# Kernel tuning notes

Measured on AMD Instinct MI355X. Metric: run time of the kernel, lower is better.

The kernel has to match this reference:

```python
import jax, jax.numpy as jnp
import numpy as np
from jax import lax

B, CIN, COUT, K, S, P, H, W = 8, 128, 256, 3, 1, 1, 64, 64


def setup_inputs() -> dict:
    key = jax.random.key(0)
    k1, k2, k3, k4, k5 = jax.random.split(key, 5)
    fan_off = CIN * K * K
    fan_dc = CIN * K * K
    return {
        "x": jax.random.normal(k1, (B, CIN, H, W), dtype=jnp.float32),
        # offset-predicting conv: Conv2d(CIN, 2*K*K, K, S, P, padding_mode='reflect')
        "w_off": jax.random.normal(k2, (2 * K * K, CIN, K, K), dtype=jnp.float32) / np.sqrt(fan_off),
        "b_off": jax.random.normal(k3, (2 * K * K,), dtype=jnp.float32) * 0.01,
        # deformable conv weights: DeformConv2d(CIN, COUT, K, S, P)
        "w_dc": jax.random.normal(k4, (COUT, CIN, K, K), dtype=jnp.float32) / np.sqrt(fan_dc),
        "b_dc": jax.random.normal(k5, (COUT,), dtype=jnp.float32) * 0.01,
    }


def _reflect_conv(x, w, b, stride, pad):
    # Conv2d with reflect padding
    xp = jnp.pad(x, ((0, 0), (0, 0), (pad, pad), (pad, pad)), mode="reflect")
    y = lax.conv_general_dilated(xp, w, (stride, stride), "VALID",
                                 dimension_numbers=("NCHW", "OIHW", "NCHW"))
    return y + b[None, :, None, None]


def _deform_conv(x, offset, w, b, k, stride, pad):
    # torchvision DeformConv2d (v1, no mask, 1 offset group)
    Bn, C, Hi, Wi = x.shape
    Ho, Wo = offset.shape[2], offset.shape[3]
    KK = k * k
    # offset layout: [B, 2*KK, Ho, Wo], interleaved (dy, dx) per kernel position
    off = offset.reshape(Bn, KK, 2, Ho, Wo)
    hb = jnp.arange(Ho, dtype=x.dtype) * stride - pad          # base rows
    wb = jnp.arange(Wo, dtype=x.dtype) * stride - pad          # base cols
    ki, kj = jnp.meshgrid(jnp.arange(k, dtype=x.dtype), jnp.arange(k, dtype=x.dtype), indexing="ij")
    ki, kj = ki.reshape(KK), kj.reshape(KK)
    # sampling locations [B, KK, Ho, Wo]
    py = off[:, :, 0] + hb[None, None, :, None] + ki[None, :, None, None]
    px = off[:, :, 1] + wb[None, None, None, :] + kj[None, :, None, None]
    y0 = jnp.floor(py)
    x0 = jnp.floor(px)
    dy = (py - y0).reshape(Bn, 1, -1)
    dx = (px - x0).reshape(Bn, 1, -1)
    y0i = y0.astype(jnp.int32)
    x0i = x0.astype(jnp.int32)
    xf = x.reshape(Bn, C, Hi * Wi)

    def gather(yi, xi):
        valid = (yi >= 0) & (yi < Hi) & (xi >= 0) & (xi < Wi)
        yc = jnp.clip(yi, 0, Hi - 1)
        xc = jnp.clip(xi, 0, Wi - 1)
        idx = (yc * Wi + xc).reshape(Bn, -1)                   # [B, KK*Ho*Wo]
        g = jax.vmap(lambda xb, ib: xb[:, ib])(xf, idx)        # [B, C, KK*Ho*Wo]
        return g * valid.reshape(Bn, 1, -1).astype(x.dtype)

    v00 = gather(y0i, x0i)
    v01 = gather(y0i, x0i + 1)
    v10 = gather(y0i + 1, x0i)
    v11 = gather(y0i + 1, x0i + 1)
    vals = (v00 * (1 - dy) * (1 - dx) + v01 * (1 - dy) * dx
            + v10 * dy * (1 - dx) + v11 * dy * dx)             # [B, C, KK*Ho*Wo]
    cols = vals.reshape(Bn, C, KK, Ho * Wo)
    out = jnp.einsum("bckl,ock->bol", cols, w.reshape(-1, C, KK))
    out = out + b[None, :, None]
    return out.reshape(Bn, -1, Ho, Wo)


def reference(x, w_off, b_off, w_dc, b_dc):
    x_offset = _reflect_conv(x, w_off, b_off, S, P)            # [B, 2*K*K, Ho, Wo]
    # torch.chunk followed by torch.concat is an identity on the offset tensor
    return _deform_conv(x, x_offset, w_dc, b_dc, K, S, P)
```

## Files before the change

### kernel.cpp

```cpp
#include <hip/hip_runtime.h>
#include <hip/hip_fp16.h>

typedef unsigned short u16;
typedef unsigned int   u32;
typedef u32   u32x2  __attribute__((ext_vector_type(2)));
typedef u32   u32x4  __attribute__((ext_vector_type(4)));
typedef short short8 __attribute__((ext_vector_type(8)));
typedef float f32x4  __attribute__((ext_vector_type(4)));
typedef _Float16 half8 __attribute__((ext_vector_type(8)));

__device__ __forceinline__ u16 f2h(float f) { return __half_as_ushort(__float2half(f)); }
__device__ __forceinline__ f32x4 mfma16(short8 a, short8 b, f32x4 c) {
  return __builtin_amdgcn_mfma_f32_16x16x32_f16(
      __builtin_bit_cast(half8, a), __builtin_bit_cast(half8, b), c, 0, 0, 0);
}
__device__ __forceinline__ __half2 h2cast(u32 u) { return __builtin_bit_cast(__half2, u); }

__global__ __launch_bounds__(256) void prep_fused(const float* __restrict__ x,
                                                  const float* __restrict__ w_dc,
                                                  const float* __restrict__ w_off,
                                                  u16* __restrict__ xh,
                                                  u16* __restrict__ Wl2,
                                                  u16* __restrict__ Wol2) {
  int bid = blockIdx.x;
  int tid = threadIdx.x;
  if (bid < 512) {
    __shared__ float tile[128][65];
    int swz = (bid & 7) * 64 + (bid >> 3);
    int b = swz >> 6, h = swz & 63;
    for (int i = 0; i < 32; ++i) {
      int c = (tid >> 6) + i * 4;
      int w = tid & 63;
      tile[c][w] = x[(((size_t)b * 128 + c) * 64 + h) * 64 + w];
    }
    __syncthreads();
    u16* dst = xh + ((size_t)(b * 64 + h) * 64) * 128;
    for (int j = 0; j < 32; ++j) {
      int c = tid & 127;
      int w = (tid >> 7) + 2 * j;
      dst[w * 128 + c] = f2h(tile[c][w]);
    }
  } else {
    int idx = (bid - 512) * 256 + tid;
    if (idx < 294912) {
      int e = idx & 7, lane = (idx >> 3) & 63, ks = (idx >> 9) & 3;
      int mt = (idx >> 11) & 15, kk = idx >> 15;
      int o = mt * 16 + (lane & 15), c = ks * 32 + (lane >> 4) * 8 + e;
      Wl2[idx] = f2h(w_dc[(o * 128 + c) * 9 + kk]);
    } else {
      int i2 = idx - 294912;
      int e = i2 & 7, lane = (i2 >> 3) & 63, ks = (i2 >> 9) & 3;
      int mt = (i2 >> 11) & 1, kk = i2 >> 12;
      int co = mt * 16 + (lane & 15), c = ks * 32 + (lane >> 4) * 8 + e;
      Wol2[i2] = (co < 18) ? f2h(w_off[(co * 128 + c) * 9 + kk]) : (u16)0;
    }
  }
}

__device__ __forceinline__ void make_entry_lds(u32x4* __restrict__ tbl, int kk,
                                               int ho, int wo, float offy, float offx) {
  int ki = kk / 3, kj = kk - ki * 3;
  float py = offy + (float)(ho + ki - 1);
  float px = offx + (float)(wo + kj - 1);
  float fy0 = floorf(py), fx0 = floorf(px);
  int y0 = (int)fy0, x0 = (int)fx0;
  float fy = py - fy0, fx = px - fx0;
  float w11 = fy * fx, w10 = fy - w11, w01 = fx - w11, w00 = 1.f - fy - fx + w11;
  bool iy0 = (y0 >= 0) & (y0 < 64), iy1 = (y0 >= -1) & (y0 < 63);
  bool ix0 = (x0 >= 0) & (x0 < 64), ix1 = (x0 >= -1) & (x0 < 63);
  int y0c = min(max(y0, 0), 63), x0c = min(max(x0, 0), 63);
  u32 addr00 = (u32)((y0c * 64 + x0c) * 128);
  u32 dx = (x0 >= 0 && x0 < 63) ? 128u : 0u;
  u32 dy = (y0 >= 0 && y0 < 63) ? 8192u : 0u;
  u32 wA = (u32)f2h((iy0 && ix0) ? w00 : 0.f) | ((u32)f2h((iy0 && ix1) ? w01 : 0.f) << 16);
  u32 wB = (u32)f2h((iy1 && ix0) ? w10 : 0.f) | ((u32)f2h((iy1 && ix1) ? w11 : 0.f) << 16);
  u32x4 ent; ent.x = addr00; ent.y = dx | (dy << 16); ent.z = wA; ent.w = wB;
  tbl[kk * 64 + wo] = ent;
}

__global__ __launch_bounds__(512, 4) void deform_fused(
    const u16* __restrict__ xh, const u16* __restrict__ Wl2,
    const u16* __restrict__ Wol2, const float* __restrict__ b_off,
    const float* __restrict__ b_dc, float* __restrict__ out) {
  union SMU {
    u16 slab[3][64][128];
    struct { u16 cols[2][64][128]; u32x4 tbl[576]; } pb;
  };
  __shared__ SMU sm;
  int bid = blockIdx.x;
  int swz = (bid & 7) * 64 + (bid >> 3);
  int b = swz >> 6, ho = swz & 63;
  int tid = threadIdx.x, lane = tid & 63, wv = tid >> 6;
  int ln15 = lane & 15, kg = lane >> 4;
  const u16* xb = xh + (size_t)b * 524288;

  int tl0 = tid >> 4;
  int tcl = (tid & 15) * 8;
  int swzc = tcl ^ ((tl0 & 7) << 3);

  {
    u32x4 st[6];
#pragma unroll
    for (int i = 0; i < 6; ++i) {
      int T = tid + i * 512;
      int r = T >> 10, w = (T >> 4) & 63, cb = (T & 15) * 8;
      int hr = ho + r - 1; hr = hr < 0 ? -hr : (hr > 63 ? 126 - hr : hr);
      st[i] = *(const u32x4*)(xb + (hr * 64 + w) * 128 + cb);
    }
#pragma unroll
    for (int i = 0; i < 6; ++i) {
      int T = tid + i * 512;
      int r = T >> 10, w = (T >> 4) & 63, cb = (T & 15) * 8;
      *(u32x4*)&sm.slab[r][w][cb ^ ((w & 7) << 3)] = st[i];
    }
  }
  __syncthreads();

  int mt = wv & 1, ntq = wv >> 1;
  int lq = ntq * 16 + ln15;
  f32x4 oacc = {0.f, 0.f, 0.f, 0.f};
  __builtin_amdgcn_s_setprio(1);
#pragma unroll
  for (int kk = 0; kk < 9; ++kk) {
    int ki = kk / 3, kj = kk - ki * 3;
    int wr = lq + kj - 1; wr = wr < 0 ? -wr : (wr > 63 ? 126 - wr : wr);
    const u16* wb = Wol2 + ((kk * 2 + mt) * 4) * 512 + lane * 8;
    int sb = (wr & 7) << 3;
#pragma unroll
    for (int ks = 0; ks < 4; ++ks) {
      short8 af = *(const short8*)(wb + ks * 512);
      short8 bf = *(const short8*)&sm.slab[ki][wr][(ks * 32 + kg * 8) ^ sb];
      oacc = mfma16(af, bf, oacc);
    }
  }
  __builtin_amdgcn_s_setprio(0);
  __syncthreads();

  {
    int wo = lq;
    if (mt == 0) {
      int kkA = 2 * kg, kkB = 2 * kg + 1;
      make_entry_lds(sm.pb.tbl, kkA, ho, wo, oacc[0] + b_off[2 * kkA], oacc[1] + b_off[2 * kkA + 1]);
      make_entry_lds(sm.pb.tbl, kkB, ho, wo, oacc[2] + b_off[2 * kkB], oacc[3] + b_off[2 * kkB + 1]);
    } else if (kg == 0) {
      make_entry_lds(sm.pb.tbl, 8, ho, wo, oacc[0] + b_off[16], oacc[1] + b_off[17]);
    }
  }
  __syncthreads();

  u32x4 gv[2][4];
  u32x4 ge[2];
  auto gissue = [&](int g) {
#pragma unroll
    for (int i = 0; i < 2; ++i) {
      int l = tl0 + i * 32;
      u32x4 e = sm.pb.tbl[g * 64 + l];
      ge[i] = e;
      const u16* p = xb + e.x + tcl;
      u32 dxv = e.y & 0xffffu, dyv = e.y >> 16;
      gv[i][0] = *(const u32x4*)p;
      gv[i][1] = *(const u32x4*)(p + dxv);
      gv[i][2] = *(const u32x4*)(p + dyv);
      gv[i][3] = *(const u32x4*)(p + dyv + dxv);
    }
  };
  auto gwrite = [&](int dbuf) {
#pragma unroll
    for (int i = 0; i < 2; ++i) {
      __half2 wA = h2cast(ge[i].z), wB = h2cast(ge[i].w);
      __half2 w00 = __half2half2(wA.x), w01 = __half2half2(wA.y);
      __half2 w10 = __half2half2(wB.x), w11 = __half2half2(wB.y);
      u32x4 pv;
#pragma unroll
      for (int wd = 0; wd < 4; ++wd) {
        __half2 r = __hmul2(h2cast(gv[i][0][wd]), w00);
        r = __hfma2(h2cast(gv[i][1][wd]), w01, r);
        r = __hfma2(h2cast(gv[i][2][wd]), w10, r);
        r = __hfma2(h2cast(gv[i][3][wd]), w11, r);
        pv[wd] = __builtin_bit_cast(u32, r);
      }
      *(u32x4*)&sm.pb.cols[dbuf][tl0 + i * 32][swzc] = pv;
    }
  };

  f32x4 acc[2][4];
#pragma unroll
  for (int m = 0; m < 2; ++m)
#pragma unroll
    for (int n = 0; n < 4; ++n) acc[m][n] = (f32x4){0.f, 0.f, 0.f, 0.f};

  gissue(0);
  gwrite(0);
  __syncthreads();

  for (int kk = 0; kk < 9; ++kk) {
    int buf = kk & 1;
    const u16* wbase = Wl2 + (size_t)((kk * 16 + wv * 2) * 4) * 512;
    short8 a[8];
#pragma unroll
    for (int ks = 0; ks < 4; ++ks) {
      a[ks]     = *(const short8*)(wbase + ks * 512 + lane * 8);
      a[4 + ks] = *(const short8*)(wbase + (4 + ks) * 512 + lane * 8);
    }
    if (kk < 8) gissue(kk + 1);
    __builtin_amdgcn_s_setprio(1);
#pragma unroll
    for (int ks = 0; ks < 4; ++ks) {
#pragma unroll
      for (int nt = 0; nt < 4; ++nt) {
        int l = nt * 16 + ln15;
        short8 bfv = *(const short8*)&sm.pb.cols[buf][l][(ks * 32 + kg * 8) ^ ((l & 7) << 3)];
        acc[0][nt] = mfma16(a[ks], bfv, acc[0][nt]);
        acc[1][nt] = mfma16(a[4 + ks], bfv, acc[1][nt]);
      }
    }
    __builtin_amdgcn_s_setprio(0);
    if (kk < 8) gwrite(buf ^ 1);
    __syncthreads();
  }

#pragma unroll
  for (int mtt = 0; mtt < 2; ++mtt) {
#pragma unroll
    for (int r = 0; r < 4; ++r) {
      int o = wv * 32 + mtt * 16 + kg * 4 + r;
      float bias = b_dc[o];
      size_t base = ((size_t)(b * 256 + o)) * 4096 + ho * 64;
#pragma unroll
      for (int nt = 0; nt < 4; ++nt) {
        out[base + nt * 16 + ln15] = acc[mtt][nt][r] + bias;
      }
    }
  }
}

extern "C" void kernel_launch(void* const* d_in, const int* in_sizes, int n_in,
                              void* d_out, int out_size, void* d_ws, size_t ws_size,
                              hipStream_t stream) {
  const float* x     = (const float*)d_in[0];
  const float* w_off = (const float*)d_in[1];
  const float* b_off = (const float*)d_in[2];
  const float* w_dc  = (const float*)d_in[3];
  const float* b_dc  = (const float*)d_in[4];
  float* out = (float*)d_out;
  char* ws = (char*)d_ws;
  u16* xh   = (u16*)ws;
  u16* Wl2  = (u16*)(ws + 8388608);
  u16* Wol2 = (u16*)(ws + 8388608 + 589824);
  prep_fused  <<<dim3(1808), dim3(256), 0, stream>>>(x, w_dc, w_off, xh, Wl2, Wol2);
  deform_fused<<<dim3(512),  dim3(512), 0, stream>>>(xh, Wl2, Wol2, b_off, b_dc, out);
}
```

Measured before the change: 47.61 us.

## Halve workgroup to 256 threads with larger per-wave MFMA tiles and compact gather table

Changes the deform kernel from 512 to 256 threads per block, so each wave now computes 64 output channels (4 M-tiles) instead of 32. This reuses each LDS B-fragment across four MFMAs, and the offset conv now handles two N-tiles per wave. The gather/interpolation pipeline is split into two half-K phases per kernel tap to bound register use. The sampling table is packed into 3 words per entry instead of 4, and the batch-major block swizzle is replaced by a simple interleave. The aim is less LDS read traffic and a smaller LDS footprint, at the cost of fewer waves per block and higher register pressure from 64 accumulators per thread.

```diff
diff --git a/kernel.cpp b/kernel.cpp
--- a/kernel.cpp
+++ b/kernel.cpp
@@ -57,8 +57,8 @@
   }
 }
 
-__device__ __forceinline__ void make_entry_lds(u32x4* __restrict__ tbl, int kk,
-                                               int ho, int wo, float offy, float offx) {
+__device__ __forceinline__ void make_entry3(u32* __restrict__ tbl, int kk,
+                                            int ho, int wo, float offy, float offx) {
   int ki = kk / 3, kj = kk - ki * 3;
   float py = offy + (float)(ho + ki - 1);
   float px = offx + (float)(wo + kj - 1);
@@ -69,27 +69,28 @@
   bool iy0 = (y0 >= 0) & (y0 < 64), iy1 = (y0 >= -1) & (y0 < 63);
   bool ix0 = (x0 >= 0) & (x0 < 64), ix1 = (x0 >= -1) & (x0 < 63);
   int y0c = min(max(y0, 0), 63), x0c = min(max(x0, 0), 63);
-  u32 addr00 = (u32)((y0c * 64 + x0c) * 128);
-  u32 dx = (x0 >= 0 && x0 < 63) ? 128u : 0u;
-  u32 dy = (y0 >= 0 && y0 < 63) ? 8192u : 0u;
+  u32 addr = (u32)((y0c * 64 + x0c) * 128);
+  u32 dxf = (x0 >= 0 && x0 < 63) ? 1u : 0u;
+  u32 dyf = (y0 >= 0 && y0 < 63) ? 1u : 0u;
   u32 wA = (u32)f2h((iy0 && ix0) ? w00 : 0.f) | ((u32)f2h((iy0 && ix1) ? w01 : 0.f) << 16);
   u32 wB = (u32)f2h((iy1 && ix0) ? w10 : 0.f) | ((u32)f2h((iy1 && ix1) ? w11 : 0.f) << 16);
-  u32x4 ent; ent.x = addr00; ent.y = dx | (dy << 16); ent.z = wA; ent.w = wB;
-  tbl[kk * 64 + wo] = ent;
-}
-
-__global__ __launch_bounds__(512, 4) void deform_fused(
+  int base = (kk * 64 + wo) * 3;
+  tbl[base]     = addr | (dxf << 20) | (dyf << 21);
+  tbl[base + 1] = wA;
+  tbl[base + 2] = wB;
+}
+
+__global__ __launch_bounds__(256, 3) void deform_fused(
     const u16* __restrict__ xh, const u16* __restrict__ Wl2,
     const u16* __restrict__ Wol2, const float* __restrict__ b_off,
     const float* __restrict__ b_dc, float* __restrict__ out) {
   union SMU {
     u16 slab[3][64][128];
-    struct { u16 cols[2][64][128]; u32x4 tbl[576]; } pb;
+    struct { u16 cols[2][64][128]; u32 tbl[1728]; } pb;
   };
   __shared__ SMU sm;
   int bid = blockIdx.x;
-  int swz = (bid & 7) * 64 + (bid >> 3);
-  int b = swz >> 6, ho = swz & 63;
+  int b = bid & 7, ho = bid >> 3;
   int tid = threadIdx.x, lane = tid & 63, wv = tid >> 6;
   int ln15 = lane & 15, kg = lane >> 4;
   const u16* xb = xh + (size_t)b * 524288;
@@ -99,75 +100,81 @@
   int swzc = tcl ^ ((tl0 & 7) << 3);
 
   {
-    u32x4 st[6];
-#pragma unroll
-    for (int i = 0; i < 6; ++i) {
-      int T = tid + i * 512;
+    u32x4 st[12];
+#pragma unroll
+    for (int i = 0; i < 12; ++i) {
+      int T = tid + i * 256;
       int r = T >> 10, w = (T >> 4) & 63, cb = (T & 15) * 8;
       int hr = ho + r - 1; hr = hr < 0 ? -hr : (hr > 63 ? 126 - hr : hr);
       st[i] = *(const u32x4*)(xb + (hr * 64 + w) * 128 + cb);
     }
 #pragma unroll
-    for (int i = 0; i < 6; ++i) {
-      int T = tid + i * 512;
+    for (int i = 0; i < 12; ++i) {
+      int T = tid + i * 256;
       int r = T >> 10, w = (T >> 4) & 63, cb = (T & 15) * 8;
       *(u32x4*)&sm.slab[r][w][cb ^ ((w & 7) << 3)] = st[i];
     }
   }
   __syncthreads();
 
-  int mt = wv & 1, ntq = wv >> 1;
-  int lq = ntq * 16 + ln15;
-  f32x4 oacc = {0.f, 0.f, 0.f, 0.f};
+  int mtA = wv & 1;
+  int ntb = (wv >> 1) * 2;
+  int lqa = ntb * 16 + ln15, lqb = (ntb + 1) * 16 + ln15;
+  f32x4 oacc0 = {0.f, 0.f, 0.f, 0.f}, oacc1 = {0.f, 0.f, 0.f, 0.f};
   __builtin_amdgcn_s_setprio(1);
 #pragma unroll
   for (int kk = 0; kk < 9; ++kk) {
     int ki = kk / 3, kj = kk - ki * 3;
-    int wr = lq + kj - 1; wr = wr < 0 ? -wr : (wr > 63 ? 126 - wr : wr);
-    const u16* wb = Wol2 + ((kk * 2 + mt) * 4) * 512 + lane * 8;
-    int sb = (wr & 7) << 3;
+    int wra = lqa + kj - 1; wra = wra < 0 ? -wra : (wra > 63 ? 126 - wra : wra);
+    int wrb = lqb + kj - 1; wrb = wrb < 0 ? -wrb : (wrb > 63 ? 126 - wrb : wrb);
+    const u16* wb = Wol2 + ((kk * 2 + mtA) * 4) * 512 + lane * 8;
+    int sba = (wra & 7) << 3, sbb = (wrb & 7) << 3;
 #pragma unroll
     for (int ks = 0; ks < 4; ++ks) {
       short8 af = *(const short8*)(wb + ks * 512);
-      short8 bf = *(const short8*)&sm.slab[ki][wr][(ks * 32 + kg * 8) ^ sb];
-      oacc = mfma16(af, bf, oacc);
+      oacc0 = mfma16(af, *(const short8*)&sm.slab[ki][wra][(ks * 32 + kg * 8) ^ sba], oacc0);
+      oacc1 = mfma16(af, *(const short8*)&sm.slab[ki][wrb][(ks * 32 + kg * 8) ^ sbb], oacc1);
     }
   }
   __builtin_amdgcn_s_setprio(0);
   __syncthreads();
 
-  {
-    int wo = lq;
-    if (mt == 0) {
-      int kkA = 2 * kg, kkB = 2 * kg + 1;
-      make_entry_lds(sm.pb.tbl, kkA, ho, wo, oacc[0] + b_off[2 * kkA], oacc[1] + b_off[2 * kkA + 1]);
-      make_entry_lds(sm.pb.tbl, kkB, ho, wo, oacc[2] + b_off[2 * kkB], oacc[3] + b_off[2 * kkB + 1]);
-    } else if (kg == 0) {
-      make_entry_lds(sm.pb.tbl, 8, ho, wo, oacc[0] + b_off[16], oacc[1] + b_off[17]);
-    }
+  if (mtA == 0) {
+    int kkA = 2 * kg, kkB = 2 * kg + 1;
+    make_entry3(sm.pb.tbl, kkA, ho, lqa, oacc0[0] + b_off[2 * kkA], oacc0[1] + b_off[2 * kkA + 1]);
+    make_entry3(sm.pb.tbl, kkB, ho, lqa, oacc0[2] + b_off[2 * kkB], oacc0[3] + b_off[2 * kkB + 1]);
+    make_entry3(sm.pb.tbl, kkA, ho, lqb, oacc1[0] + b_off[2 * kkA], oacc1[1] + b_off[2 * kkA + 1]);
+    make_entry3(sm.pb.tbl, kkB, ho, lqb, oacc1[2] + b_off[2 * kkB], oacc1[3] + b_off[2 * kkB + 1]);
+  } else if (kg == 0) {
+    make_entry3(sm.pb.tbl, 8, ho, lqa, oacc0[0] + b_off[16], oacc0[1] + b_off[17]);
+    make_entry3(sm.pb.tbl, 8, ho, lqb, oacc1[0] + b_off[16], oacc1[1] + b_off[17]);
   }
   __syncthreads();
 
   u32x4 gv[2][4];
-  u32x4 ge[2];
-  auto gissue = [&](int g) {
+  u32 gwAv[2], gwBv[2];
+  auto gissue2 = [&](int g, int i0) {
 #pragma unroll
     for (int i = 0; i < 2; ++i) {
-      int l = tl0 + i * 32;
-      u32x4 e = sm.pb.tbl[g * 64 + l];
-      ge[i] = e;
-      const u16* p = xb + e.x + tcl;
-      u32 dxv = e.y & 0xffffu, dyv = e.y >> 16;
+      int l = tl0 + (i0 + i) * 16;
+      int base3 = (g * 64 + l) * 3;
+      u32 e0 = sm.pb.tbl[base3];
+      gwAv[i] = sm.pb.tbl[base3 + 1];
+      gwBv[i] = sm.pb.tbl[base3 + 2];
+      const u16* p = xb + (e0 & 0xFFFFFu) + tcl;
+      u32 dxv = ((e0 >> 20) & 1) << 7;
+      u32 dyv = ((e0 >> 21) & 1) << 13;
       gv[i][0] = *(const u32x4*)p;
       gv[i][1] = *(const u32x4*)(p + dxv);
       gv[i][2] = *(const u32x4*)(p + dyv);
       gv[i][3] = *(const u32x4*)(p + dyv + dxv);
     }
   };
-  auto gwrite = [&](int dbuf) {
+  auto gwrite2 = [&](int dbuf, int i0) {
 #pragma unroll
     for (int i = 0; i < 2; ++i) {
-      __half2 wA = h2cast(ge[i].z), wB = h2cast(ge[i].w);
+      int l = tl0 + (i0 + i) * 16;
+      __half2 wA = h2cast(gwAv[i]), wB = h2cast(gwBv[i]);
       __half2 w00 = __half2half2(wA.x), w01 = __half2half2(wA.y);
       __half2 w10 = __half2half2(wB.x), w11 = __half2half2(wB.y);
       u32x4 pv;
@@ -179,56 +186,78 @@
         r = __hfma2(h2cast(gv[i][3][wd]), w11, r);
         pv[wd] = __builtin_bit_cast(u32, r);
       }
-      *(u32x4*)&sm.pb.cols[dbuf][tl0 + i * 32][swzc] = pv;
+      *(u32x4*)&sm.pb.cols[dbuf][l][swzc] = pv;
     }
   };
 
-  f32x4 acc[2][4];
-#pragma unroll
-  for (int m = 0; m < 2; ++m)
+  f32x4 acc[4][4];
+#pragma unroll
+  for (int m = 0; m < 4; ++m)
 #pragma unroll
     for (int n = 0; n < 4; ++n) acc[m][n] = (f32x4){0.f, 0.f, 0.f, 0.f};
 
-  gissue(0);
-  gwrite(0);
-  __syncthreads();
-
+  gissue2(0, 0); gwrite2(0, 0);
+  gissue2(0, 2); gwrite2(0, 2);
+  __syncthreads();
+
+  int swzb = (ln15 & 7) << 3;
   for (int kk = 0; kk < 9; ++kk) {
     int buf = kk & 1;
-    const u16* wbase = Wl2 + (size_t)((kk * 16 + wv * 2) * 4) * 512;
-    short8 a[8];
-#pragma unroll
-    for (int ks = 0; ks < 4; ++ks) {
-      a[ks]     = *(const short8*)(wbase + ks * 512 + lane * 8);
-      a[4 + ks] = *(const short8*)(wbase + (4 + ks) * 512 + lane * 8);
-    }
-    if (kk < 8) gissue(kk + 1);
+    bool more = kk < 8;
+    const u16* wbase = Wl2 + (size_t)((kk * 16 + wv * 4) * 4) * 512 + lane * 8;
+    short8 a0[4][2];
+#pragma unroll
+    for (int mt = 0; mt < 4; ++mt)
+#pragma unroll
+      for (int k2 = 0; k2 < 2; ++k2)
+        a0[mt][k2] = *(const short8*)(wbase + (mt * 4 + k2) * 512);
+    if (more) gissue2(kk + 1, 0);
     __builtin_amdgcn_s_setprio(1);
 #pragma unroll
-    for (int ks = 0; ks < 4; ++ks) {
+    for (int k2 = 0; k2 < 2; ++k2) {
 #pragma unroll
       for (int nt = 0; nt < 4; ++nt) {
-        int l = nt * 16 + ln15;
-        short8 bfv = *(const short8*)&sm.pb.cols[buf][l][(ks * 32 + kg * 8) ^ ((l & 7) << 3)];
-        acc[0][nt] = mfma16(a[ks], bfv, acc[0][nt]);
-        acc[1][nt] = mfma16(a[4 + ks], bfv, acc[1][nt]);
+        short8 bf = *(const short8*)&sm.pb.cols[buf][nt * 16 + ln15][(k2 * 32 + kg * 8) ^ swzb];
+#pragma unroll
+        for (int mt = 0; mt < 4; ++mt)
+          acc[mt][nt] = mfma16(a0[mt][k2], bf, acc[mt][nt]);
       }
     }
     __builtin_amdgcn_s_setprio(0);
-    if (kk < 8) gwrite(buf ^ 1);
+    if (more) gwrite2(buf ^ 1, 0);
+    short8 a1[4][2];
+#pragma unroll
+    for (int mt = 0; mt < 4; ++mt)
+#pragma unroll
+      for (int k2 = 0; k2 < 2; ++k2)
+        a1[mt][k2] = *(const short8*)(wbase + (mt * 4 + 2 + k2) * 512);
+    if (more) gissue2(kk + 1, 2);
+    __builtin_amdgcn_s_setprio(1);
+#pragma unroll
+    for (int k2 = 0; k2 < 2; ++k2) {
+#pragma unroll
+      for (int nt = 0; nt < 4; ++nt) {
+        short8 bf = *(const short8*)&sm.pb.cols[buf][nt * 16 + ln15][((k2 + 2) * 32 + kg * 8) ^ swzb];
+#pragma unroll
+        for (int mt = 0; mt < 4; ++mt)
+          acc[mt][nt] = mfma16(a1[mt][k2], bf, acc[mt][nt]);
+      }
+    }
+    __builtin_amdgcn_s_setprio(0);
+    if (more) gwrite2(buf ^ 1, 2);
     __syncthreads();
   }
 
 #pragma unroll
-  for (int mtt = 0; mtt < 2; ++mtt) {
+  for (int mt = 0; mt < 4; ++mt) {
 #pragma unroll
     for (int r = 0; r < 4; ++r) {
-      int o = wv * 32 + mtt * 16 + kg * 4 + r;
+      int o = wv * 64 + mt * 16 + kg * 4 + r;
       float bias = b_dc[o];
       size_t base = ((size_t)(b * 256 + o)) * 4096 + ho * 64;
 #pragma unroll
       for (int nt = 0; nt < 4; ++nt) {
-        out[base + nt * 16 + ln15] = acc[mtt][nt][r] + bias;
+        out[base + nt * 16 + ln15] = acc[mt][nt][r] + bias;
       }
     }
   }
@@ -248,5 +277,5 @@
   u16* Wl2  = (u16*)(ws + 8388608);
   u16* Wol2 = (u16*)(ws + 8388608 + 589824);
   prep_fused  <<<dim3(1808), dim3(256), 0, stream>>>(x, w_dc, w_off, xh, Wl2, Wol2);
-  deform_fused<<<dim3(512),  dim3(512), 0, stream>>>(xh, Wl2, Wol2, b_off, b_dc, out);
-}
+  deform_fused<<<dim3(512),  dim3(256), 0, stream>>>(xh, Wl2, Wol2, b_off, b_dc, out);
+}
```

After: 55.25 us. 1.16x slower.

## Split each output row across two 256-thread blocks with 32-column tiles

Applied to the files above, without the earlier changes.

The fused deformable-conv kernel now runs 1024 blocks of 256 threads. Each block handles half an output row (32 columns) and stages only a 3x36 reflect-padded slab instead of the full 3x64 rows. Each wave now computes 64 output channels by 32 columns. The bilinear gather/blend is split into two halves interleaved with the MFMA k-steps, to lower register pressure and raise block count and occupancy. In exchange, each block loads the deform weights again for half the work and recomputes a 2-column halo in the offset conv.

```diff
diff --git a/kernel.cpp b/kernel.cpp
--- a/kernel.cpp
+++ b/kernel.cpp
@@ -15,6 +15,7 @@
       __builtin_bit_cast(half8, a), __builtin_bit_cast(half8, b), c, 0, 0, 0);
 }
 __device__ __forceinline__ __half2 h2cast(u32 u) { return __builtin_bit_cast(__half2, u); }
+__device__ __forceinline__ int refl(int v) { return v < 0 ? -v : (v > 63 ? 126 - v : v); }
 
 __global__ __launch_bounds__(256) void prep_fused(const float* __restrict__ x,
                                                   const float* __restrict__ w_dc,
@@ -58,10 +59,11 @@
 }
 
 __device__ __forceinline__ void make_entry_lds(u32x4* __restrict__ tbl, int kk,
-                                               int ho, int wo, float offy, float offx) {
+                                               int ho, int wo_g, int lql,
+                                               float offy, float offx) {
   int ki = kk / 3, kj = kk - ki * 3;
   float py = offy + (float)(ho + ki - 1);
-  float px = offx + (float)(wo + kj - 1);
+  float px = offx + (float)(wo_g + kj - 1);
   float fy0 = floorf(py), fx0 = floorf(px);
   int y0 = (int)fy0, x0 = (int)fx0;
   float fy = py - fy0, fx = px - fx0;
@@ -75,161 +77,165 @@
   u32 wA = (u32)f2h((iy0 && ix0) ? w00 : 0.f) | ((u32)f2h((iy0 && ix1) ? w01 : 0.f) << 16);
   u32 wB = (u32)f2h((iy1 && ix0) ? w10 : 0.f) | ((u32)f2h((iy1 && ix1) ? w11 : 0.f) << 16);
   u32x4 ent; ent.x = addr00; ent.y = dx | (dy << 16); ent.z = wA; ent.w = wB;
-  tbl[kk * 64 + wo] = ent;
-}
-
-__global__ __launch_bounds__(512, 4) void deform_fused(
+  tbl[kk * 32 + lql] = ent;
+}
+
+__global__ __launch_bounds__(256, 4) void deform_fused(
     const u16* __restrict__ xh, const u16* __restrict__ Wl2,
     const u16* __restrict__ Wol2, const float* __restrict__ b_off,
     const float* __restrict__ b_dc, float* __restrict__ out) {
   union SMU {
-    u16 slab[3][64][128];
-    struct { u16 cols[2][64][128]; u32x4 tbl[576]; } pb;
+    u16 slab[3][36][128];
+    struct { u16 cols[2][32][128]; u32x4 tbl[288]; } pb;
   };
   __shared__ SMU sm;
   int bid = blockIdx.x;
-  int swz = (bid & 7) * 64 + (bid >> 3);
-  int b = swz >> 6, ho = swz & 63;
+  int b = bid & 7, t = bid >> 3;
+  int ho = t >> 1, l0 = (t & 1) * 32;
   int tid = threadIdx.x, lane = tid & 63, wv = tid >> 6;
   int ln15 = lane & 15, kg = lane >> 4;
   const u16* xb = xh + (size_t)b * 524288;
 
+  {
+    u32x4 st[7];
+#pragma unroll
+    for (int i = 0; i < 7; ++i) {
+      int T = tid + i * 256;
+      if (T < 1728) {
+        int r = T / 576, rem = T - r * 576;
+        int j = rem >> 4, cb = (rem & 15) * 8;
+        int hr = refl(ho + r - 1);
+        int w = refl(l0 + j - 1);
+        st[i] = *(const u32x4*)(xb + (hr * 64 + w) * 128 + cb);
+      }
+    }
+#pragma unroll
+    for (int i = 0; i < 7; ++i) {
+      int T = tid + i * 256;
+      if (T < 1728) {
+        int r = T / 576, rem = T - r * 576;
+        int j = rem >> 4, cb = (rem & 15) * 8;
+        *(u32x4*)&sm.slab[r][j][cb ^ ((j & 7) << 3)] = st[i];
+      }
+    }
+  }
+  __syncthreads();
+
+  int mtA = wv & 1, ntA = wv >> 1;
+  int lql = ntA * 16 + ln15;
+  f32x4 oacc = {0.f, 0.f, 0.f, 0.f};
+  __builtin_amdgcn_s_setprio(1);
+#pragma unroll
+  for (int kk = 0; kk < 9; ++kk) {
+    int ki = kk / 3, kj = kk - ki * 3;
+    int j = lql + kj;
+    const u16* wb = Wol2 + ((kk * 2 + mtA) * 4) * 512 + lane * 8;
+    int sbj = (j & 7) << 3;
+#pragma unroll
+    for (int ks = 0; ks < 4; ++ks) {
+      short8 af = *(const short8*)(wb + ks * 512);
+      short8 bf = *(const short8*)&sm.slab[ki][j][(ks * 32 + kg * 8) ^ sbj];
+      oacc = mfma16(af, bf, oacc);
+    }
+  }
+  __builtin_amdgcn_s_setprio(0);
+  __syncthreads();
+
+  if (mtA == 0) {
+    int kkA = 2 * kg, kkB = 2 * kg + 1;
+    make_entry_lds(sm.pb.tbl, kkA, ho, l0 + lql, lql, oacc[0] + b_off[2 * kkA], oacc[1] + b_off[2 * kkA + 1]);
+    make_entry_lds(sm.pb.tbl, kkB, ho, l0 + lql, lql, oacc[2] + b_off[2 * kkB], oacc[3] + b_off[2 * kkB + 1]);
+  } else if (kg == 0) {
+    make_entry_lds(sm.pb.tbl, 8, ho, l0 + lql, lql, oacc[0] + b_off[16], oacc[1] + b_off[17]);
+  }
+  __syncthreads();
+
   int tl0 = tid >> 4;
   int tcl = (tid & 15) * 8;
   int swzc = tcl ^ ((tl0 & 7) << 3);
 
-  {
-    u32x4 st[6];
-#pragma unroll
-    for (int i = 0; i < 6; ++i) {
-      int T = tid + i * 512;
-      int r = T >> 10, w = (T >> 4) & 63, cb = (T & 15) * 8;
-      int hr = ho + r - 1; hr = hr < 0 ? -hr : (hr > 63 ? 126 - hr : hr);
-      st[i] = *(const u32x4*)(xb + (hr * 64 + w) * 128 + cb);
-    }
-#pragma unroll
-    for (int i = 0; i < 6; ++i) {
-      int T = tid + i * 512;
-      int r = T >> 10, w = (T >> 4) & 63, cb = (T & 15) * 8;
-      *(u32x4*)&sm.slab[r][w][cb ^ ((w & 7) << 3)] = st[i];
-    }
-  }
-  __syncthreads();
-
-  int mt = wv & 1, ntq = wv >> 1;
-  int lq = ntq * 16 + ln15;
-  f32x4 oacc = {0.f, 0.f, 0.f, 0.f};
-  __builtin_amdgcn_s_setprio(1);
-#pragma unroll
-  for (int kk = 0; kk < 9; ++kk) {
-    int ki = kk / 3, kj = kk - ki * 3;
-    int wr = lq + kj - 1; wr = wr < 0 ? -wr : (wr > 63 ? 126 - wr : wr);
-    const u16* wb = Wol2 + ((kk * 2 + mt) * 4) * 512 + lane * 8;
-    int sb = (wr & 7) << 3;
-#pragma unroll
-    for (int ks = 0; ks < 4; ++ks) {
-      short8 af = *(const short8*)(wb + ks * 512);
-      short8 bf = *(const short8*)&sm.slab[ki][wr][(ks * 32 + kg * 8) ^ sb];
-      oacc = mfma16(af, bf, oacc);
-    }
-  }
-  __builtin_amdgcn_s_setprio(0);
-  __syncthreads();
-
-  {
-    int wo = lq;
-    if (mt == 0) {
-      int kkA = 2 * kg, kkB = 2 * kg + 1;
-      make_entry_lds(sm.pb.tbl, kkA, ho, wo, oacc[0] + b_off[2 * kkA], oacc[1] + b_off[2 * kkA + 1]);
-      make_entry_lds(sm.pb.tbl, kkB, ho, wo, oacc[2] + b_off[2 * kkB], oacc[3] + b_off[2 * kkB + 1]);
-    } else if (kg == 0) {
-      make_entry_lds(sm.pb.tbl, 8, ho, wo, oacc[0] + b_off[16], oacc[1] + b_off[17]);
-    }
-  }
-  __syncthreads();
-
-  u32x4 gv[2][4];
-  u32x4 ge[2];
-  auto gissue = [&](int g) {
-#pragma unroll
-    for (int i = 0; i < 2; ++i) {
-      int l = tl0 + i * 32;
-      u32x4 e = sm.pb.tbl[g * 64 + l];
-      ge[i] = e;
-      const u16* p = xb + e.x + tcl;
-      u32 dxv = e.y & 0xffffu, dyv = e.y >> 16;
-      gv[i][0] = *(const u32x4*)p;
-      gv[i][1] = *(const u32x4*)(p + dxv);
-      gv[i][2] = *(const u32x4*)(p + dyv);
-      gv[i][3] = *(const u32x4*)(p + dyv + dxv);
-    }
+  u32x4 gv[4];
+  u32 gwAv, gwBv;
+  auto gissue = [&](int g, int h) {
+    int l = tl0 + h * 16;
+    u32x4 e = sm.pb.tbl[g * 32 + l];
+    gwAv = e.z; gwBv = e.w;
+    const u16* p = xb + e.x + tcl;
+    u32 dxv = e.y & 0xffffu, dyv = e.y >> 16;
+    gv[0] = *(const u32x4*)p;
+    gv[1] = *(const u32x4*)(p + dxv);
+    gv[2] = *(const u32x4*)(p + dyv);
+    gv[3] = *(const u32x4*)(p + dyv + dxv);
   };
-  auto gwrite = [&](int dbuf) {
-#pragma unroll
-    for (int i = 0; i < 2; ++i) {
-      __half2 wA = h2cast(ge[i].z), wB = h2cast(ge[i].w);
-      __half2 w00 = __half2half2(wA.x), w01 = __half2half2(wA.y);
-      __half2 w10 = __half2half2(wB.x), w11 = __half2half2(wB.y);
-      u32x4 pv;
-#pragma unroll
-      for (int wd = 0; wd < 4; ++wd) {
-        __half2 r = __hmul2(h2cast(gv[i][0][wd]), w00);
-        r = __hfma2(h2cast(gv[i][1][wd]), w01, r);
-        r = __hfma2(h2cast(gv[i][2][wd]), w10, r);
-        r = __hfma2(h2cast(gv[i][3][wd]), w11, r);
-        pv[wd] = __builtin_bit_cast(u32, r);
-      }
-      *(u32x4*)&sm.pb.cols[dbuf][tl0 + i * 32][swzc] = pv;
-    }
+  auto gwrite = [&](int dbuf, int h) {
+    int l = tl0 + h * 16;
+    __half2 wA = h2cast(gwAv), wB = h2cast(gwBv);
+    __half2 w00 = __half2half2(wA.x), w01 = __half2half2(wA.y);
+    __half2 w10 = __half2half2(wB.x), w11 = __half2half2(wB.y);
+    u32x4 pv;
+#pragma unroll
+    for (int wd = 0; wd < 4; ++wd) {
+      __half2 r = __hmul2(h2cast(gv[0][wd]), w00);
+      r = __hfma2(h2cast(gv[1][wd]), w01, r);
+      r = __hfma2(h2cast(gv[2][wd]), w10, r);
+      r = __hfma2(h2cast(gv[3][wd]), w11, r);
+      pv[wd] = __builtin_bit_cast(u32, r);
+    }
+    *(u32x4*)&sm.pb.cols[dbuf][l][swzc] = pv;
   };
 
-  f32x4 acc[2][4];
-#pragma unroll
-  for (int m = 0; m < 2; ++m)
-#pragma unroll
-    for (int n = 0; n < 4; ++n) acc[m][n] = (f32x4){0.f, 0.f, 0.f, 0.f};
-
-  gissue(0);
-  gwrite(0);
-  __syncthreads();
-
+  f32x4 acc[4][2];
+#pragma unroll
+  for (int m = 0; m < 4; ++m) {
+    acc[m][0] = (f32x4){0.f, 0.f, 0.f, 0.f};
+    acc[m][1] = (f32x4){0.f, 0.f, 0.f, 0.f};
+  }
+
+  gissue(0, 0); gwrite(0, 0);
+  gissue(0, 1); gwrite(0, 1);
+  __syncthreads();
+
+  int swzb = (ln15 & 7) << 3;
   for (int kk = 0; kk < 9; ++kk) {
     int buf = kk & 1;
-    const u16* wbase = Wl2 + (size_t)((kk * 16 + wv * 2) * 4) * 512;
-    short8 a[8];
-#pragma unroll
-    for (int ks = 0; ks < 4; ++ks) {
-      a[ks]     = *(const short8*)(wbase + ks * 512 + lane * 8);
-      a[4 + ks] = *(const short8*)(wbase + (4 + ks) * 512 + lane * 8);
-    }
-    if (kk < 8) gissue(kk + 1);
-    __builtin_amdgcn_s_setprio(1);
-#pragma unroll
-    for (int ks = 0; ks < 4; ++ks) {
-#pragma unroll
-      for (int nt = 0; nt < 4; ++nt) {
-        int l = nt * 16 + ln15;
-        short8 bfv = *(const short8*)&sm.pb.cols[buf][l][(ks * 32 + kg * 8) ^ ((l & 7) << 3)];
-        acc[0][nt] = mfma16(a[ks], bfv, acc[0][nt]);
-        acc[1][nt] = mfma16(a[4 + ks], bfv, acc[1][nt]);
+    bool more = kk < 8;
+    const u16* wbase = Wl2 + (size_t)kk * 32768 + lane * 8;
+#pragma unroll
+    for (int h = 0; h < 2; ++h) {
+      short8 a[4][2];
+#pragma unroll
+      for (int mt = 0; mt < 4; ++mt)
+#pragma unroll
+        for (int k2 = 0; k2 < 2; ++k2)
+          a[mt][k2] = *(const short8*)(wbase + (size_t)(((wv * 4 + mt) * 4) + h * 2 + k2) * 512);
+      if (more) gissue(kk + 1, h);
+      __builtin_amdgcn_s_setprio(1);
+#pragma unroll
+      for (int k2 = 0; k2 < 2; ++k2) {
+        int ks = h * 2 + k2;
+#pragma unroll
+        for (int nt = 0; nt < 2; ++nt) {
+          short8 bf = *(const short8*)&sm.pb.cols[buf][nt * 16 + ln15][(ks * 32 + kg * 8) ^ swzb];
+#pragma unroll
+          for (int mt = 0; mt < 4; ++mt)
+            acc[mt][nt] = mfma16(a[mt][k2], bf, acc[mt][nt]);
+        }
       }
-    }
-    __builtin_amdgcn_s_setprio(0);
-    if (kk < 8) gwrite(buf ^ 1);
+      __builtin_amdgcn_s_setprio(0);
+      if (more) gwrite(buf ^ 1, h);
+    }
     __syncthreads();
   }
 
 #pragma unroll
-  for (int mtt = 0; mtt < 2; ++mtt) {
+  for (int mt = 0; mt < 4; ++mt) {
 #pragma unroll
     for (int r = 0; r < 4; ++r) {
-      int o = wv * 32 + mtt * 16 + kg * 4 + r;
+      int o = wv * 64 + mt * 16 + kg * 4 + r;
       float bias = b_dc[o];
-      size_t base = ((size_t)(b * 256 + o)) * 4096 + ho * 64;
-#pragma unroll
-      for (int nt = 0; nt < 4; ++nt) {
-        out[base + nt * 16 + ln15] = acc[mtt][nt][r] + bias;
-      }
+      size_t base = ((size_t)(b * 256 + o)) * 4096 + ho * 64 + l0;
+      out[base + ln15]      = acc[mt][0][r] + bias;
+      out[base + 16 + ln15] = acc[mt][1][r] + bias;
     }
   }
 }
@@ -248,5 +254,5 @@
   u16* Wl2  = (u16*)(ws + 8388608);
   u16* Wol2 = (u16*)(ws + 8388608 + 589824);
   prep_fused  <<<dim3(1808), dim3(256), 0, stream>>>(x, w_dc, w_off, xh, Wl2, Wol2);
-  deform_fused<<<dim3(512),  dim3(512), 0, stream>>>(xh, Wl2, Wol2, b_off, b_dc, out);
-}
+  deform_fused<<<dim3(1024), dim3(256), 0, stream>>>(xh, Wl2, Wol2, b_off, b_dc, out);
+}
```

Result: slower. 53.65 us (+12.7%).

## Deepen gather prefetch to two stages ahead and change block-to-tile mapping

Applied to the files above, without the earlier changes.

Restructures the deformable gather pipeline so the bilinear-combine write for the next tap runs before the MFMA loop, and the global gathers are issued two kernel positions ahead instead of one. This gives the gather loads a full iteration of MFMA work to hide behind. The block index mapping also changes: consecutive blocks now cover different batches at the same row rather than the earlier swizzle, which alters L2 locality. Register pressure rises because the prefetched values stay live across a whole iteration, which could hurt occupancy under the 512x4 launch bounds.

```diff
diff --git a/kernel.cpp b/kernel.cpp
--- a/kernel.cpp
+++ b/kernel.cpp
@@ -15,6 +15,7 @@
       __builtin_bit_cast(half8, a), __builtin_bit_cast(half8, b), c, 0, 0, 0);
 }
 __device__ __forceinline__ __half2 h2cast(u32 u) { return __builtin_bit_cast(__half2, u); }
+__device__ __forceinline__ int refl(int v) { return v < 0 ? -v : (v > 63 ? 126 - v : v); }
 
 __global__ __launch_bounds__(256) void prep_fused(const float* __restrict__ x,
                                                   const float* __restrict__ w_dc,
@@ -88,23 +89,18 @@
   };
   __shared__ SMU sm;
   int bid = blockIdx.x;
-  int swz = (bid & 7) * 64 + (bid >> 3);
-  int b = swz >> 6, ho = swz & 63;
+  int b = bid & 7, ho = bid >> 3;
   int tid = threadIdx.x, lane = tid & 63, wv = tid >> 6;
   int ln15 = lane & 15, kg = lane >> 4;
   const u16* xb = xh + (size_t)b * 524288;
 
-  int tl0 = tid >> 4;
-  int tcl = (tid & 15) * 8;
-  int swzc = tcl ^ ((tl0 & 7) << 3);
-
   {
     u32x4 st[6];
 #pragma unroll
     for (int i = 0; i < 6; ++i) {
       int T = tid + i * 512;
       int r = T >> 10, w = (T >> 4) & 63, cb = (T & 15) * 8;
-      int hr = ho + r - 1; hr = hr < 0 ? -hr : (hr > 63 ? 126 - hr : hr);
+      int hr = refl(ho + r - 1);
       st[i] = *(const u32x4*)(xb + (hr * 64 + w) * 128 + cb);
     }
 #pragma unroll
@@ -116,46 +112,47 @@
   }
   __syncthreads();
 
-  int mt = wv & 1, ntq = wv >> 1;
-  int lq = ntq * 16 + ln15;
+  int mtA = wv & 1, ntA = wv >> 1;
+  int lq = ntA * 16 + ln15;
   f32x4 oacc = {0.f, 0.f, 0.f, 0.f};
   __builtin_amdgcn_s_setprio(1);
 #pragma unroll
   for (int kk = 0; kk < 9; ++kk) {
     int ki = kk / 3, kj = kk - ki * 3;
-    int wr = lq + kj - 1; wr = wr < 0 ? -wr : (wr > 63 ? 126 - wr : wr);
-    const u16* wb = Wol2 + ((kk * 2 + mt) * 4) * 512 + lane * 8;
-    int sb = (wr & 7) << 3;
+    int j = refl(lq + kj - 1);
+    const u16* wb = Wol2 + ((kk * 2 + mtA) * 4) * 512 + lane * 8;
+    int sbj = (j & 7) << 3;
 #pragma unroll
     for (int ks = 0; ks < 4; ++ks) {
       short8 af = *(const short8*)(wb + ks * 512);
-      short8 bf = *(const short8*)&sm.slab[ki][wr][(ks * 32 + kg * 8) ^ sb];
+      short8 bf = *(const short8*)&sm.slab[ki][j][(ks * 32 + kg * 8) ^ sbj];
       oacc = mfma16(af, bf, oacc);
     }
   }
   __builtin_amdgcn_s_setprio(0);
   __syncthreads();
 
-  {
-    int wo = lq;
-    if (mt == 0) {
-      int kkA = 2 * kg, kkB = 2 * kg + 1;
-      make_entry_lds(sm.pb.tbl, kkA, ho, wo, oacc[0] + b_off[2 * kkA], oacc[1] + b_off[2 * kkA + 1]);
-      make_entry_lds(sm.pb.tbl, kkB, ho, wo, oacc[2] + b_off[2 * kkB], oacc[3] + b_off[2 * kkB + 1]);
-    } else if (kg == 0) {
-      make_entry_lds(sm.pb.tbl, 8, ho, wo, oacc[0] + b_off[16], oacc[1] + b_off[17]);
-    }
-  }
-  __syncthreads();
+  if (mtA == 0) {
+    int kkA = 2 * kg, kkB = 2 * kg + 1;
+    make_entry_lds(sm.pb.tbl, kkA, ho, lq, oacc[0] + b_off[2 * kkA], oacc[1] + b_off[2 * kkA + 1]);
+    make_entry_lds(sm.pb.tbl, kkB, ho, lq, oacc[2] + b_off[2 * kkB], oacc[3] + b_off[2 * kkB + 1]);
+  } else if (kg == 0) {
+    make_entry_lds(sm.pb.tbl, 8, ho, lq, oacc[0] + b_off[16], oacc[1] + b_off[17]);
+  }
+  __syncthreads();
+
+  int tl0 = tid >> 4;
+  int tcl = (tid & 15) * 8;
+  int swzc = tcl ^ ((tl0 & 7) << 3);
 
   u32x4 gv[2][4];
-  u32x4 ge[2];
+  u32 gwAv[2], gwBv[2];
   auto gissue = [&](int g) {
 #pragma unroll
     for (int i = 0; i < 2; ++i) {
       int l = tl0 + i * 32;
       u32x4 e = sm.pb.tbl[g * 64 + l];
-      ge[i] = e;
+      gwAv[i] = e.z; gwBv[i] = e.w;
       const u16* p = xb + e.x + tcl;
       u32 dxv = e.y & 0xffffu, dyv = e.y >> 16;
       gv[i][0] = *(const u32x4*)p;
@@ -167,7 +164,8 @@
   auto gwrite = [&](int dbuf) {
 #pragma unroll
     for (int i = 0; i < 2; ++i) {
-      __half2 wA = h2cast(ge[i].z), wB = h2cast(ge[i].w);
+      int l = tl0 + i * 32;
+      __half2 wA = h2cast(gwAv[i]), wB = h2cast(gwBv[i]);
       __half2 w00 = __half2half2(wA.x), w01 = __half2half2(wA.y);
       __half2 w10 = __half2half2(wB.x), w11 = __half2half2(wB.y);
       u32x4 pv;
@@ -179,7 +177,7 @@
         r = __hfma2(h2cast(gv[i][3][wd]), w11, r);
         pv[wd] = __builtin_bit_cast(u32, r);
       }
-      *(u32x4*)&sm.pb.cols[dbuf][tl0 + i * 32][swzc] = pv;
+      *(u32x4*)&sm.pb.cols[dbuf][l][swzc] = pv;
     }
   };
 
@@ -189,46 +187,47 @@
 #pragma unroll
     for (int n = 0; n < 4; ++n) acc[m][n] = (f32x4){0.f, 0.f, 0.f, 0.f};
 
-  gissue(0);
-  gwrite(0);
-  __syncthreads();
-
+  gissue(0); gwrite(0);
+  gissue(1);
+  __syncthreads();
+
+  int swzb = (ln15 & 7) << 3;
   for (int kk = 0; kk < 9; ++kk) {
-    int buf = kk & 1;
-    const u16* wbase = Wl2 + (size_t)((kk * 16 + wv * 2) * 4) * 512;
-    short8 a[8];
+    int cur = kk & 1;
+    const u16* wbase = Wl2 + (size_t)kk * 32768 + lane * 8;
+    short8 a[2][4];
+#pragma unroll
+    for (int mt = 0; mt < 2; ++mt)
+#pragma unroll
+      for (int ks = 0; ks < 4; ++ks)
+        a[mt][ks] = *(const short8*)(wbase + (size_t)(((wv * 2 + mt) * 4) + ks) * 512);
+    if (kk < 8) gwrite(cur ^ 1);
+    if (kk < 7) gissue(kk + 2);
+    __builtin_amdgcn_s_setprio(1);
 #pragma unroll
     for (int ks = 0; ks < 4; ++ks) {
-      a[ks]     = *(const short8*)(wbase + ks * 512 + lane * 8);
-      a[4 + ks] = *(const short8*)(wbase + (4 + ks) * 512 + lane * 8);
-    }
-    if (kk < 8) gissue(kk + 1);
-    __builtin_amdgcn_s_setprio(1);
-#pragma unroll
-    for (int ks = 0; ks < 4; ++ks) {
 #pragma unroll
       for (int nt = 0; nt < 4; ++nt) {
-        int l = nt * 16 + ln15;
-        short8 bfv = *(const short8*)&sm.pb.cols[buf][l][(ks * 32 + kg * 8) ^ ((l & 7) << 3)];
-        acc[0][nt] = mfma16(a[ks], bfv, acc[0][nt]);
-        acc[1][nt] = mfma16(a[4 + ks], bfv, acc[1][nt]);
+        short8 bf = *(const short8*)&sm.pb.cols[cur][nt * 16 + ln15][(ks * 32 + kg * 8) ^ swzb];
+#pragma unroll
+        for (int mt = 0; mt < 2; ++mt)
+          acc[mt][nt] = mfma16(a[mt][ks], bf, acc[mt][nt]);
       }
     }
     __builtin_amdgcn_s_setprio(0);
-    if (kk < 8) gwrite(buf ^ 1);
     __syncthreads();
   }
 
 #pragma unroll
-  for (int mtt = 0; mtt < 2; ++mtt) {
+  for (int mt = 0; mt < 2; ++mt) {
 #pragma unroll
     for (int r = 0; r < 4; ++r) {
-      int o = wv * 32 + mtt * 16 + kg * 4 + r;
+      int o = wv * 32 + mt * 16 + kg * 4 + r;
       float bias = b_dc[o];
       size_t base = ((size_t)(b * 256 + o)) * 4096 + ho * 64;
 #pragma unroll
       for (int nt = 0; nt < 4; ++nt) {
-        out[base + nt * 16 + ln15] = acc[mtt][nt][r] + bias;
+        out[base + nt * 16 + ln15] = acc[mt][nt][r] + bias;
       }
     }
   }
```

After: 47.04 us. About the same (-1.2%).
